# Optimization experiments

Measured on AMD Instinct MI355X. Metric: run time of the kernel, lower is better.

The kernel has to match this reference:

```python
import jax, jax.numpy as jnp
import numpy as np

B, T, S, A, H = 64, 1000, 96, 32, 256
INP = S + A  # 128


def setup_inputs() -> dict:
    key = jax.random.key(0)
    ks = jax.random.split(key, 20)
    def xavier(k, shape):
        fan_in, fan_out = shape[0], shape[1]
        lim = jnp.sqrt(6.0 / (fan_in + fan_out))
        return jax.random.uniform(k, shape, jnp.float32, -lim, lim)
    return {
        "state": jax.random.normal(ks[0], (B, T, S), jnp.float32),
        "action": jax.random.normal(ks[1], (B, T, A), jnp.float32),
        "hn": jnp.zeros((1, B, H), jnp.float32),
        # branch 1 params
        "fc11_w": xavier(ks[2], (INP, H)),
        "fc11_b": jnp.zeros((H,), jnp.float32),
        "W_hh1": xavier(ks[3], (H, H)),
        "W_ih1": xavier(ks[4], (H, H)),
        "b_hh1": jax.random.uniform(ks[5], (H,), jnp.float32),
        "b_ih1": jax.random.uniform(ks[6], (H,), jnp.float32),
        "fc12_w": xavier(ks[7], (H, 1)),
        "fc12_b": jnp.zeros((1,), jnp.float32),
        # branch 2 params
        "fc21_w": xavier(ks[8], (INP, H)),
        "fc21_b": jnp.zeros((H,), jnp.float32),
        "W_hh2": xavier(ks[9], (H, H)),
        "W_ih2": xavier(ks[10], (H, H)),
        "b_hh2": jax.random.uniform(ks[11], (H,), jnp.float32),
        "b_ih2": jax.random.uniform(ks[12], (H,), jnp.float32),
        "fc22_w": xavier(ks[13], (H, 1)),
        "fc22_b": jnp.zeros((1,), jnp.float32),
    }


def _rnn_branch(x, h0, W_hh, W_ih, b_hh, b_ih):
    # x: [B, T, H] (post input projection + relu); h0: [B, H]
    bias = b_hh + b_ih
    def step(h, x_t):
        h_next = jax.nn.sigmoid(h @ W_hh + x_t @ W_ih + bias)
        return h_next, h_next
    xs = jnp.swapaxes(x, 0, 1)  # [T, B, H]
    _, hs = jax.lax.scan(step, h0, xs)
    return jnp.swapaxes(hs, 0, 1)  # [B, T, H]


def reference(state, action, hn, fc11_w, fc11_b, W_hh1, W_ih1, b_hh1, b_ih1,
              fc12_w, fc12_b, fc21_w, fc21_b, W_hh2, W_ih2, b_hh2, b_ih2,
              fc22_w, fc22_b):
    x = jnp.concatenate((state, action), axis=-1)  # [B, T, INP]
    h0 = hn[0]  # squeeze(0) -> [B, H]

    x1 = jax.nn.relu(x @ fc11_w + fc11_b)
    rnn1 = _rnn_branch(x1, h0, W_hh1, W_ih1, b_hh1, b_ih1)
    q1 = rnn1 @ fc12_w + fc12_b  # [B, T, 1]

    x2 = jax.nn.relu(x @ fc21_w + fc21_b)
    rnn2 = _rnn_branch(x2, h0, W_hh2, W_ih2, b_hh2, b_ih2)
    q2 = rnn2 @ fc22_w + fc22_b  # [B, T, 1]

    return (q1, q2)
```

## Files before the change

### kernel.cpp

```cpp
#include <hip/hip_runtime.h>
#include <math.h>


typedef _Float16 half2_t __attribute__((ext_vector_type(2)));
typedef __attribute__((ext_vector_type(8))) short bf16x8;
typedef __attribute__((ext_vector_type(4))) float f32x4;

__device__ __forceinline__ float fdot2(half2_t a, half2_t b, float c) {
#if __has_builtin(__builtin_amdgcn_fdot2)
    return __builtin_amdgcn_fdot2(a, b, c, false);
#else
    return c + (float)a[0] * (float)b[0] + (float)a[1] * (float)b[1];
#endif
}

__device__ __forceinline__ short f2bf(float f) {
    unsigned u = __builtin_bit_cast(unsigned, f);
    return (short)((u + 0x7FFFu + ((u >> 16) & 1u)) >> 16);
}

__device__ __forceinline__ void barrier_lds() {
    __asm__ __volatile__("s_waitcnt lgkmcnt(0)" ::: "memory");
    __builtin_amdgcn_s_barrier();
}

__global__ __launch_bounds__(256, 1)
void prep_kernel(const float* __restrict__ fc11_w, const float* __restrict__ W_ih1,
                 const float* __restrict__ fc21_w, const float* __restrict__ W_ih2,
                 short* __restrict__ tab)
{
    const int e    = blockIdx.x * 256 + threadIdx.x;
    const int lane = e & 63;
    const int q = lane >> 4, m = lane & 15;
    const float* W;
    int k0, n;
    if (e < 8192) {
        int t_ = e >> 6;
        int ks = t_ & 3, nt = (t_ >> 2) & 15, br = t_ >> 6;
        W = br ? fc21_w : fc11_w;
        k0 = ks * 32 + q * 8; n = nt * 16 + m;
    } else {
        int t_ = (e - 8192) >> 6;
        int ks = t_ & 7, nt = (t_ >> 3) & 15, br = t_ >> 7;
        W = br ? W_ih2 : W_ih1;
        k0 = ks * 32 + q * 8; n = nt * 16 + m;
    }
    bf16x8 v;
#pragma unroll
    for (int j = 0; j < 8; ++j) v[j] = f2bf(W[(size_t)(k0 + j) * 256 + n]);
    ((bf16x8*)tab)[e] = v;
}

__global__ __launch_bounds__(256, 2)
void ff_kernel(const float* __restrict__ state,
               const float* __restrict__ action,
               const float* __restrict__ fc11_b, const float* __restrict__ fc21_b,
               const float* __restrict__ b_hh1, const float* __restrict__ b_ih1,
               const float* __restrict__ b_hh2, const float* __restrict__ b_ih2,
               const short* __restrict__ tab,
               _Float16* __restrict__ pre_out)
{
    __shared__ short X1[128 * 264];

    const int tile = blockIdx.x % 500;
    const int br   = blockIdx.x / 500;
    const int tid  = threadIdx.x;
    const int w    = tid >> 6;
    const int lane = tid & 63;
    const int q = lane >> 4, m = lane & 15;
    const int row0 = tile * 128;

    const float* ba = br ? fc21_b : fc11_b;
    const float* bh = br ? b_hh2 : b_hh1;
    const float* bi = br ? b_ih2 : b_ih1;
    const bf16x8* tG1 = (const bf16x8*)tab + (size_t)br * 4096;
    const bf16x8* tG2 = (const bf16x8*)tab + 8192 + (size_t)br * 8192;

    float ba_v[16], bb_v[16];
#pragma unroll
    for (int nt = 0; nt < 16; ++nt) {
        int c = nt * 16 + m;
        ba_v[nt] = ba[c];
        bb_v[nt] = bh[c] + bi[c];
    }

    bf16x8 af[2][4];
#pragma unroll
    for (int mt = 0; mt < 2; ++mt) {
        const int rw = row0 + 64 * mt + 16 * w + m;
#pragma unroll
        for (int ks = 0; ks < 4; ++ks) {
            int k0 = ks * 32 + q * 8;
            const float* src = (k0 < 96) ? (state  + (size_t)rw * 96 + k0)
                                         : (action + (size_t)rw * 32 + (k0 - 96));
            float4 x0 = *(const float4*)src;
            float4 x1 = *(const float4*)(src + 4);
            bf16x8 a;
            a[0] = f2bf(x0.x); a[1] = f2bf(x0.y); a[2] = f2bf(x0.z); a[3] = f2bf(x0.w);
            a[4] = f2bf(x1.x); a[5] = f2bf(x1.y); a[6] = f2bf(x1.z); a[7] = f2bf(x1.w);
            af[mt][ks] = a;
        }
    }

#pragma unroll 4
    for (int nt = 0; nt < 16; ++nt) {
        bf16x8 bf[4];
#pragma unroll
        for (int ks = 0; ks < 4; ++ks) bf[ks] = tG1[(nt * 4 + ks) * 64 + lane];
#pragma unroll
        for (int mt = 0; mt < 2; ++mt) {
            f32x4 acc = {0.f, 0.f, 0.f, 0.f};
#pragma unroll
            for (int ks = 0; ks < 4; ++ks)
                acc = __builtin_amdgcn_mfma_f32_16x16x32_bf16(af[mt][ks], bf[ks], acc, 0, 0, 0);
#pragma unroll
            for (int r = 0; r < 4; ++r) {
                float v = acc[r] + ba_v[nt];
                v = v > 0.f ? v : 0.f;
                X1[(64 * mt + 16 * w + q * 4 + r) * 264 + nt * 16 + m] = f2bf(v);
            }
        }
    }

    bf16x8 a2[2][8];
#pragma unroll
    for (int mt = 0; mt < 2; ++mt)
#pragma unroll
        for (int ks = 0; ks < 8; ++ks)
            a2[mt][ks] = *(const bf16x8*)&X1[(64 * mt + 16 * w + m) * 264 + ks * 32 + q * 8];

    _Float16* pre = pre_out + (size_t)br * 64000u * 256u;
#pragma unroll 2
    for (int nt = 0; nt < 16; ++nt) {
        bf16x8 bg[8];
#pragma unroll
        for (int ks = 0; ks < 8; ++ks) bg[ks] = tG2[(nt * 8 + ks) * 64 + lane];
#pragma unroll
        for (int mt = 0; mt < 2; ++mt) {
            f32x4 acc = {0.f, 0.f, 0.f, 0.f};
#pragma unroll
            for (int ks = 0; ks < 8; ++ks)
                acc = __builtin_amdgcn_mfma_f32_16x16x32_bf16(a2[mt][ks], bg[ks], acc, 0, 0, 0);
#pragma unroll
            for (int r = 0; r < 4; ++r) {
                float v = acc[r] + bb_v[nt];
                pre[(size_t)(row0 + 64 * mt + 16 * w + q * 4 + r) * 256 + nt * 16 + m] = (_Float16)v;
            }
        }
    }
}

__global__ __launch_bounds__(512, 2)
void rnn_kernel(const _Float16* __restrict__ pre_all,
                const float* __restrict__ hn,
                const float* __restrict__ W_hh1,
                const float* __restrict__ W_hh2,
                _Float16* __restrict__ h_out)
{
    __shared__ _Float16 hbuf[256];
    __shared__ float part[2][8][256];

    const int wg = blockIdx.x;
    const int br = wg >> 6;
    const int b  = wg & 63;
    const float* Whh = br ? W_hh2 : W_hh1;
    const _Float16* pre = pre_all + ((size_t)br * 64000u + (size_t)b * 1000u) * 256u;
    _Float16* hg = h_out + ((size_t)br * 64000u + (size_t)b * 1000u) * 256u;

    const int t    = threadIdx.x;
    const int w    = t >> 6;
    const int lane = t & 63;
    const int k0   = w * 32;
    const int c0   = lane * 4;
    const int cr   = (w << 5) + (lane & 31);

    unsigned whb[4][16];
#pragma unroll
    for (int i = 0; i < 16; ++i) {
        float4 lo = *(const float4*)(Whh + (size_t)(k0 + 2 * i) * 256 + c0);
        float4 hi = *(const float4*)(Whh + (size_t)(k0 + 2 * i + 1) * 256 + c0);
        whb[0][i] = __builtin_bit_cast(unsigned, half2_t{(_Float16)lo.x, (_Float16)hi.x});
        whb[1][i] = __builtin_bit_cast(unsigned, half2_t{(_Float16)lo.y, (_Float16)hi.y});
        whb[2][i] = __builtin_bit_cast(unsigned, half2_t{(_Float16)lo.z, (_Float16)hi.z});
        whb[3][i] = __builtin_bit_cast(unsigned, half2_t{(_Float16)lo.w, (_Float16)hi.w});
    }
#pragma unroll
    for (int c = 0; c < 4; ++c)
#pragma unroll
        for (int i = 0; i < 16; ++i)
            __asm__ __volatile__("" : "+v"(whb[c][i]));

    if (t < 256) hbuf[t] = (_Float16)hn[b * 256 + t];
    barrier_lds();

    float pre_c = (float)pre[cr];
    float pre_n = (float)pre[256 + cr];

    for (int tt = 0; tt < 1000; ++tt) {
        const int t2 = (tt + 2 < 1000) ? (tt + 2) : 999;
        const float pre_n2 = (float)pre[(size_t)t2 * 256 + cr];

        const float4* hb = (const float4*)&hbuf[k0];
        float s0 = 0.f, s1 = 0.f, s2 = 0.f, s3 = 0.f;
#pragma unroll
        for (int k = 0; k < 4; ++k) {
            float4 v = hb[k];
            const half2_t* hh = (const half2_t*)&v;
#define WH(c, idx) __builtin_bit_cast(half2_t, whb[c][idx])
#pragma unroll
            for (int p = 0; p < 4; ++p) {
                s0 = fdot2(hh[p], WH(0, 4 * k + p), s0);
                s1 = fdot2(hh[p], WH(1, 4 * k + p), s1);
                s2 = fdot2(hh[p], WH(2, 4 * k + p), s2);
                s3 = fdot2(hh[p], WH(3, 4 * k + p), s3);
            }
#undef WH
        }
        const int pp = tt & 1;
        *(float4*)&part[pp][w][c0] = float4{s0, s1, s2, s3};
        barrier_lds();

        if (lane < 32) {
            const float* pc = &part[pp][0][cr];
            float z = ((pc[0 * 256] + pc[1 * 256]) + (pc[2 * 256] + pc[3 * 256]))
                    + ((pc[4 * 256] + pc[5 * 256]) + (pc[6 * 256] + pc[7 * 256]))
                    + pre_c;
            const float h = 1.0f / (1.0f + __expf(-z));
            const _Float16 h16 = (_Float16)h;
            hbuf[cr] = h16;
            hg[(size_t)tt * 256 + cr] = h16;
        }

        pre_c = pre_n;
        pre_n = pre_n2;
    }
}

__global__ __launch_bounds__(256, 2)
void q_kernel(const _Float16* __restrict__ h_all,
              const float* __restrict__ fc12_w, const float* __restrict__ fc12_b,
              const float* __restrict__ fc22_w, const float* __restrict__ fc22_b,
              float* __restrict__ out)
{
    const int n  = blockIdx.x * 256 + threadIdx.x;
    const int br = (n >= 64000);
    const float* qwp = br ? fc22_w : fc12_w;
    const float  qb  = br ? fc22_b[0] : fc12_b[0];

    half2_t qw[128];
#pragma unroll
    for (int i = 0; i < 128; ++i)
        qw[i] = half2_t{(_Float16)qwp[2 * i], (_Float16)qwp[2 * i + 1]};

    const float4* hr = (const float4*)(h_all + (size_t)n * 256u);
    float s0 = qb, s1 = 0.f, s2 = 0.f, s3 = 0.f;
#pragma unroll
    for (int k = 0; k < 32; ++k) {
        float4 v = hr[k];
        const half2_t* hh = (const half2_t*)&v;
        s0 = fdot2(hh[0], qw[4 * k + 0], s0);
        s1 = fdot2(hh[1], qw[4 * k + 1], s1);
        s2 = fdot2(hh[2], qw[4 * k + 2], s2);
        s3 = fdot2(hh[3], qw[4 * k + 3], s3);
    }
    out[n] = (s0 + s1) + (s2 + s3);
}

extern "C" void kernel_launch(void* const* d_in, const int* in_sizes, int n_in,
                              void* d_out, int out_size, void* d_ws, size_t ws_size,
                              hipStream_t stream)
{
    const float* state  = (const float*)d_in[0];
    const float* action = (const float*)d_in[1];
    const float* hn     = (const float*)d_in[2];
    const float* fc11_w = (const float*)d_in[3];
    const float* fc11_b = (const float*)d_in[4];
    const float* W_hh1  = (const float*)d_in[5];
    const float* W_ih1  = (const float*)d_in[6];
    const float* b_hh1  = (const float*)d_in[7];
    const float* b_ih1  = (const float*)d_in[8];
    const float* fc12_w = (const float*)d_in[9];
    const float* fc12_b = (const float*)d_in[10];
    const float* fc21_w = (const float*)d_in[11];
    const float* fc21_b = (const float*)d_in[12];
    const float* W_hh2  = (const float*)d_in[13];
    const float* W_ih2  = (const float*)d_in[14];
    const float* b_hh2  = (const float*)d_in[15];
    const float* b_ih2  = (const float*)d_in[16];
    const float* fc22_w = (const float*)d_in[17];
    const float* fc22_b = (const float*)d_in[18];

    _Float16* pre = (_Float16*)d_ws;
    _Float16* hbg = (_Float16*)d_ws + 32768000u;
    short* tab = (short*)((char*)d_ws + 130678784u);

    prep_kernel<<<96, 256, 0, stream>>>(fc11_w, W_ih1, fc21_w, W_ih2, tab);
    ff_kernel<<<1000, 256, 0, stream>>>(state, action,
                                        fc11_b, fc21_b, b_hh1, b_ih1,
                                        b_hh2, b_ih2, tab, pre);
    rnn_kernel<<<128, 512, 0, stream>>>(pre, hn, W_hh1, W_hh2, hbg);
    q_kernel<<<500, 256, 0, stream>>>(hbg, fc12_w, fc12_b, fc22_w, fc22_b,
                                      (float*)d_out);
}
```

Before: 764.0 us.

## Batch 16 sequences per workgroup with MFMA recurrence and fused Q head

Recasts the recurrent step as bf16 MFMA matrix products over 16 batch rows per workgroup. W_hh is pre-packed into fragments by the prep kernel and held in accumulation registers, and h is double-buffered in LDS. The Q output projection is folded into the recurrence through shuffles and a small LDS reduction. This removes the full hidden-state write to global memory and the separate q_kernel. In exchange, only 8 workgroups run, and the hidden state is carried in bf16 instead of fp16, which lowers precision.

```diff
diff --git a/kernel.cpp b/kernel.cpp
--- a/kernel.cpp
+++ b/kernel.cpp
@@ -6,14 +6,6 @@
 typedef __attribute__((ext_vector_type(8))) short bf16x8;
 typedef __attribute__((ext_vector_type(4))) float f32x4;
 
-__device__ __forceinline__ float fdot2(half2_t a, half2_t b, float c) {
-#if __has_builtin(__builtin_amdgcn_fdot2)
-    return __builtin_amdgcn_fdot2(a, b, c, false);
-#else
-    return c + (float)a[0] * (float)b[0] + (float)a[1] * (float)b[1];
-#endif
-}
-
 __device__ __forceinline__ short f2bf(float f) {
     unsigned u = __builtin_bit_cast(unsigned, f);
     return (short)((u + 0x7FFFu + ((u >> 16) & 1u)) >> 16);
@@ -27,6 +19,7 @@
 __global__ __launch_bounds__(256, 1)
 void prep_kernel(const float* __restrict__ fc11_w, const float* __restrict__ W_ih1,
                  const float* __restrict__ fc21_w, const float* __restrict__ W_ih2,
+                 const float* __restrict__ W_hh1, const float* __restrict__ W_hh2,
                  short* __restrict__ tab)
 {
     const int e    = blockIdx.x * 256 + threadIdx.x;
@@ -39,11 +32,16 @@
         int ks = t_ & 3, nt = (t_ >> 2) & 15, br = t_ >> 6;
         W = br ? fc21_w : fc11_w;
         k0 = ks * 32 + q * 8; n = nt * 16 + m;
-    } else {
+    } else if (e < 24576) {
         int t_ = (e - 8192) >> 6;
         int ks = t_ & 7, nt = (t_ >> 3) & 15, br = t_ >> 7;
         W = br ? W_ih2 : W_ih1;
         k0 = ks * 32 + q * 8; n = nt * 16 + m;
+    } else {
+        int f = (e - 24576) >> 6;
+        int kt = f & 7, mt = (f >> 3) & 3, w = (f >> 5) & 3, br = f >> 7;
+        W = br ? W_hh2 : W_hh1;
+        k0 = kt * 32 + q * 8; n = w * 64 + mt * 16 + m;
     }
     bf16x8 v;
 #pragma unroll
@@ -150,120 +148,120 @@
     }
 }
 
-__global__ __launch_bounds__(512, 2)
+__global__ __launch_bounds__(256)
+__attribute__((amdgpu_waves_per_eu(1, 1)))
 void rnn_kernel(const _Float16* __restrict__ pre_all,
                 const float* __restrict__ hn,
-                const float* __restrict__ W_hh1,
-                const float* __restrict__ W_hh2,
-                _Float16* __restrict__ h_out)
+                const short* __restrict__ tabA,
+                const float* __restrict__ fc12_w, const float* __restrict__ fc12_b,
+                const float* __restrict__ fc22_w, const float* __restrict__ fc22_b,
+                float* __restrict__ out)
 {
-    __shared__ _Float16 hbuf[256];
-    __shared__ float part[2][8][256];
-
-    const int wg = blockIdx.x;
-    const int br = wg >> 6;
-    const int b  = wg & 63;
-    const float* Whh = br ? W_hh2 : W_hh1;
-    const _Float16* pre = pre_all + ((size_t)br * 64000u + (size_t)b * 1000u) * 256u;
-    _Float16* hg = h_out + ((size_t)br * 64000u + (size_t)b * 1000u) * 256u;
-
-    const int t    = threadIdx.x;
-    const int w    = t >> 6;
-    const int lane = t & 63;
-    const int k0   = w * 32;
-    const int c0   = lane * 4;
-    const int cr   = (w << 5) + (lane & 31);
-
-    unsigned whb[4][16];
-#pragma unroll
-    for (int i = 0; i < 16; ++i) {
-        float4 lo = *(const float4*)(Whh + (size_t)(k0 + 2 * i) * 256 + c0);
-        float4 hi = *(const float4*)(Whh + (size_t)(k0 + 2 * i + 1) * 256 + c0);
-        whb[0][i] = __builtin_bit_cast(unsigned, half2_t{(_Float16)lo.x, (_Float16)hi.x});
-        whb[1][i] = __builtin_bit_cast(unsigned, half2_t{(_Float16)lo.y, (_Float16)hi.y});
-        whb[2][i] = __builtin_bit_cast(unsigned, half2_t{(_Float16)lo.z, (_Float16)hi.z});
-        whb[3][i] = __builtin_bit_cast(unsigned, half2_t{(_Float16)lo.w, (_Float16)hi.w});
-    }
-#pragma unroll
-    for (int c = 0; c < 4; ++c)
-#pragma unroll
-        for (int i = 0; i < 16; ++i)
-            __asm__ __volatile__("" : "+v"(whb[c][i]));
-
-    if (t < 256) hbuf[t] = (_Float16)hn[b * 256 + t];
-    barrier_lds();
-
-    float pre_c = (float)pre[cr];
-    float pre_n = (float)pre[256 + cr];
-
-    for (int tt = 0; tt < 1000; ++tt) {
-        const int t2 = (tt + 2 < 1000) ? (tt + 2) : 999;
-        const float pre_n2 = (float)pre[(size_t)t2 * 256 + cr];
-
-        const float4* hb = (const float4*)&hbuf[k0];
-        float s0 = 0.f, s1 = 0.f, s2 = 0.f, s3 = 0.f;
-#pragma unroll
-        for (int k = 0; k < 4; ++k) {
-            float4 v = hb[k];
-            const half2_t* hh = (const half2_t*)&v;
-#define WH(c, idx) __builtin_bit_cast(half2_t, whb[c][idx])
-#pragma unroll
-            for (int p = 0; p < 4; ++p) {
-                s0 = fdot2(hh[p], WH(0, 4 * k + p), s0);
-                s1 = fdot2(hh[p], WH(1, 4 * k + p), s1);
-                s2 = fdot2(hh[p], WH(2, 4 * k + p), s2);
-                s3 = fdot2(hh[p], WH(3, 4 * k + p), s3);
-            }
-#undef WH
-        }
-        const int pp = tt & 1;
-        *(float4*)&part[pp][w][c0] = float4{s0, s1, s2, s3};
-        barrier_lds();
-
-        if (lane < 32) {
-            const float* pc = &part[pp][0][cr];
-            float z = ((pc[0 * 256] + pc[1 * 256]) + (pc[2 * 256] + pc[3 * 256]))
-                    + ((pc[4 * 256] + pc[5 * 256]) + (pc[6 * 256] + pc[7 * 256]))
-                    + pre_c;
-            const float h = 1.0f / (1.0f + __expf(-z));
-            const _Float16 h16 = (_Float16)h;
-            hbuf[cr] = h16;
-            hg[(size_t)tt * 256 + cr] = h16;
-        }
-
-        pre_c = pre_n;
-        pre_n = pre_n2;
-    }
-}
-
-__global__ __launch_bounds__(256, 2)
-void q_kernel(const _Float16* __restrict__ h_all,
-              const float* __restrict__ fc12_w, const float* __restrict__ fc12_b,
-              const float* __restrict__ fc22_w, const float* __restrict__ fc22_b,
-              float* __restrict__ out)
-{
-    const int n  = blockIdx.x * 256 + threadIdx.x;
-    const int br = (n >= 64000);
+    __shared__ short hlds[2][8][4][16][8];
+    __shared__ float qpart[2][4][16];
+
+    const int g    = blockIdx.x;
+    const int br   = g >> 2;
+    const int gb   = g & 3;
+    const int tid  = threadIdx.x;
+    const int wv   = tid >> 6;
+    const int lane = tid & 63;
+    const int q    = lane >> 4;
+    const int mm   = lane & 15;
+    const int cl   = gb * 16 + mm;
+
+    const bf16x8* tA = (const bf16x8*)tabA;
+    bf16x8 af[4][8];
+#pragma unroll
+    for (int mt = 0; mt < 4; ++mt)
+#pragma unroll
+        for (int kt = 0; kt < 8; ++kt)
+            af[mt][kt] = tA[(size_t)((((br * 4 + wv) * 4 + mt) * 8) + kt) * 64 + lane];
+#pragma unroll
+    for (int mt = 0; mt < 4; ++mt)
+#pragma unroll
+        for (int kt = 0; kt < 8; ++kt)
+            __asm__ __volatile__("" : "+a"(af[mt][kt]));
+
     const float* qwp = br ? fc22_w : fc12_w;
     const float  qb  = br ? fc22_b[0] : fc12_b[0];
-
-    half2_t qw[128];
-#pragma unroll
-    for (int i = 0; i < 128; ++i)
-        qw[i] = half2_t{(_Float16)qwp[2 * i], (_Float16)qwp[2 * i + 1]};
-
-    const float4* hr = (const float4*)(h_all + (size_t)n * 256u);
-    float s0 = qb, s1 = 0.f, s2 = 0.f, s3 = 0.f;
-#pragma unroll
-    for (int k = 0; k < 32; ++k) {
-        float4 v = hr[k];
-        const half2_t* hh = (const half2_t*)&v;
-        s0 = fdot2(hh[0], qw[4 * k + 0], s0);
-        s1 = fdot2(hh[1], qw[4 * k + 1], s1);
-        s2 = fdot2(hh[2], qw[4 * k + 2], s2);
-        s3 = fdot2(hh[3], qw[4 * k + 3], s3);
-    }
-    out[n] = (s0 + s1) + (s2 + s3);
+    f32x4 qw[4];
+#pragma unroll
+    for (int mt = 0; mt < 4; ++mt)
+        qw[mt] = *(const f32x4*)&qwp[wv * 64 + mt * 16 + q * 4];
+
+    for (int idx = tid; idx < 16 * 256; idx += 256) {
+        int m = idx >> 8, j = idx & 255;
+        hlds[0][j >> 5][(j >> 3) & 3][m][j & 7] = f2bf(hn[(gb * 16 + m) * 256 + j]);
+    }
+
+    const _Float16* pre = pre_all + ((size_t)br * 64000 + (size_t)cl * 1000) * 256;
+    const int joff = wv * 64 + q * 4;
+    uint2 pc[4], pn[4];
+#pragma unroll
+    for (int mt = 0; mt < 4; ++mt) {
+        pc[mt] = *(const uint2*)(pre + joff + mt * 16);
+        pn[mt] = *(const uint2*)(pre + 256 + joff + mt * 16);
+    }
+
+    barrier_lds();
+
+    for (int tt = 0; tt < 1000; ++tt) {
+        const int pp = tt & 1;
+        const int t2 = (tt + 2 < 1000) ? (tt + 2) : 999;
+        uint2 pn2[4];
+#pragma unroll
+        for (int mt = 0; mt < 4; ++mt)
+            pn2[mt] = *(const uint2*)(pre + (size_t)t2 * 256 + joff + mt * 16);
+
+        bf16x8 bh[8];
+#pragma unroll
+        for (int kt = 0; kt < 8; ++kt)
+            bh[kt] = *(const bf16x8*)&hlds[pp][kt][q][mm][0];
+
+        f32x4 z[4];
+#pragma unroll
+        for (int mt = 0; mt < 4; ++mt) {
+            half2_t lo = __builtin_bit_cast(half2_t, pc[mt].x);
+            half2_t hi = __builtin_bit_cast(half2_t, pc[mt].y);
+            z[mt] = f32x4{(float)lo[0], (float)lo[1], (float)hi[0], (float)hi[1]};
+        }
+#pragma unroll
+        for (int kt = 0; kt < 8; ++kt)
+#pragma unroll
+            for (int mt = 0; mt < 4; ++mt)
+                z[mt] = __builtin_amdgcn_mfma_f32_16x16x32_bf16(af[mt][kt], bh[kt], z[mt], 0, 0, 0);
+
+        float qp = 0.f;
+#pragma unroll
+        for (int mt = 0; mt < 4; ++mt) {
+            float h0 = 1.0f / (1.0f + __expf(-z[mt].x));
+            float h1 = 1.0f / (1.0f + __expf(-z[mt].y));
+            float h2 = 1.0f / (1.0f + __expf(-z[mt].z));
+            float h3 = 1.0f / (1.0f + __expf(-z[mt].w));
+            qp += h0 * qw[mt].x + h1 * qw[mt].y + h2 * qw[mt].z + h3 * qw[mt].w;
+            unsigned d0 = (unsigned)(unsigned short)f2bf(h0) |
+                          ((unsigned)(unsigned short)f2bf(h1) << 16);
+            unsigned d1 = (unsigned)(unsigned short)f2bf(h2) |
+                          ((unsigned)(unsigned short)f2bf(h3) << 16);
+            const int j0m = wv * 64 + mt * 16 + q * 4;
+            *(uint2*)&hlds[pp ^ 1][j0m >> 5][(j0m >> 3) & 3][mm][j0m & 7] = uint2{d0, d1};
+        }
+        qp += __shfl_xor(qp, 16, 64);
+        qp += __shfl_xor(qp, 32, 64);
+        if (lane < 16) qpart[pp][wv][mm] = qp;
+
+        barrier_lds();
+
+        if (wv == 0 && lane < 16) {
+            float qv = qpart[pp][0][mm] + qpart[pp][1][mm] +
+                       qpart[pp][2][mm] + qpart[pp][3][mm] + qb;
+            out[(size_t)br * 64000 + (size_t)cl * 1000 + tt] = qv;
+        }
+
+#pragma unroll
+        for (int mt = 0; mt < 4; ++mt) { pc[mt] = pn[mt]; pn[mt] = pn2[mt]; }
+    }
 }
 
 extern "C" void kernel_launch(void* const* d_in, const int* in_sizes, int n_in,
@@ -291,14 +289,14 @@
     const float* fc22_b = (const float*)d_in[18];
 
     _Float16* pre = (_Float16*)d_ws;
-    _Float16* hbg = (_Float16*)d_ws + 32768000u;
-    short* tab = (short*)((char*)d_ws + 130678784u);
-
-    prep_kernel<<<96, 256, 0, stream>>>(fc11_w, W_ih1, fc21_w, W_ih2, tab);
+    short* tab = (short*)((char*)d_ws + 65536000u);
+
+    prep_kernel<<<160, 256, 0, stream>>>(fc11_w, W_ih1, fc21_w, W_ih2,
+                                         W_hh1, W_hh2, tab);
     ff_kernel<<<1000, 256, 0, stream>>>(state, action,
                                         fc11_b, fc21_b, b_hh1, b_ih1,
                                         b_hh2, b_ih2, tab, pre);
-    rnn_kernel<<<128, 512, 0, stream>>>(pre, hn, W_hh1, W_hh2, hbg);
-    q_kernel<<<500, 256, 0, stream>>>(hbg, fc12_w, fc12_b, fc22_w, fc22_b,
+    rnn_kernel<<<8, 256, 0, stream>>>(pre, hn, tab + 24576 * 8,
+                                      fc12_w, fc12_b, fc22_w, fc22_b,
                                       (float*)d_out);
 }
```

New measurement: 1.356 ms. 1.77x slower.
